# Optimization experiments

Hardware: AMD Instinct MI355X
Metric: run time of the kernel (lower is better)

The kernel has to match this reference:

```python
import math
import jax, jax.numpy as jnp
import numpy as np

N_HEAD = 16


def setup_inputs() -> dict:
    key = jax.random.key(0)
    ks = jax.random.split(key, 6)
    B, T, C = 4, 2048, 1024
    hs = C // N_HEAD
    block_size = 2048
    x = jax.random.normal(ks[0], (B, T, C), dtype=jnp.float32)
    c_attn_w = jax.random.normal(ks[1], (C, 3 * C), dtype=jnp.float32) * 0.02
    c_attn_b = jnp.zeros((3 * C,), dtype=jnp.float32)
    c_proj_w = jax.random.normal(ks[2], (C, C), dtype=jnp.float32) * (0.02 * (2 * 24) ** -0.5)
    c_proj_b = jnp.zeros((C,), dtype=jnp.float32)
    wpe = jax.random.normal(ks[3], (block_size, hs), dtype=jnp.float32) * 0.02
    return {"x": x, "c_attn_w": c_attn_w, "c_attn_b": c_attn_b,
            "c_proj_w": c_proj_w, "c_proj_b": c_proj_b, "wpe": wpe}


def reference(x, c_attn_w, c_attn_b, c_proj_w, c_proj_b, wpe):
    B, T, C = x.shape
    hs = C // N_HEAD
    # fused QKV projection
    qkv = x @ c_attn_w + c_attn_b            # [B, T, 3C]
    q, k, v = jnp.split(qkv, 3, axis=-1)
    pos_emb = wpe[:T]                        # [T, hs]
    # NOTE: faithful to original — raw reshape (not transpose) before the add
    q = (q.reshape(B, N_HEAD, T, hs) + pos_emb).reshape(B, T, N_HEAD, hs)
    k = (k.reshape(B, N_HEAD, T, hs) + pos_emb).reshape(B, T, N_HEAD, hs)
    v = v.reshape(B, T, N_HEAD, hs)
    # vanilla causal attention
    qt = jnp.transpose(q, (0, 2, 1, 3))      # [B, H, T, hs]
    kt = jnp.transpose(k, (0, 2, 3, 1))      # [B, H, hs, T]
    vt = jnp.transpose(v, (0, 2, 1, 3))      # [B, H, T, hs]
    att = qt @ kt / math.sqrt(hs)            # [B, H, T, T]
    causal = jnp.tril(jnp.ones((T, T), dtype=bool))
    att = jnp.where(causal, att, float('-inf'))
    att = jax.nn.softmax(att, axis=-1)
    y = att @ vt                             # [B, H, T, hs]
    y = jnp.transpose(y, (0, 2, 1, 3)).reshape(B, T, C)
    return y @ c_proj_w + c_proj_b
```

## Files before the change

### kernel.cpp

```cpp
#include <hip/hip_runtime.h>

typedef __attribute__((ext_vector_type(8))) short s16x8;
typedef __attribute__((ext_vector_type(4))) float f32x4;
typedef __attribute__((ext_vector_type(4))) unsigned short u16x4;

#define AS1 __attribute__((address_space(1)))
#define AS3 __attribute__((address_space(3)))

__device__ __forceinline__ unsigned short f2bf(float f) {
    union { float f; unsigned u; } c; c.f = f;
    return (unsigned short)((c.u + 0x7FFFu + ((c.u >> 16) & 1u)) >> 16);
}

__global__ void k_f32_to_bf16(const float* __restrict__ src,
                              unsigned short* __restrict__ dst, int n8) {
    int idx = blockIdx.x * 256 + threadIdx.x;
    int stride = gridDim.x * 256;
    for (int i = idx; i < n8; i += stride) {
        const float4* s = (const float4*)src + (size_t)i * 2;
        float4 a = s[0], b = s[1];
        s16x8 o;
        o[0] = (short)f2bf(a.x); o[1] = (short)f2bf(a.y);
        o[2] = (short)f2bf(a.z); o[3] = (short)f2bf(a.w);
        o[4] = (short)f2bf(b.x); o[5] = (short)f2bf(b.y);
        o[6] = (short)f2bf(b.z); o[7] = (short)f2bf(b.w);
        *((s16x8*)dst + i) = o;
    }
}

__global__ __launch_bounds__(256) void k_transpose_bf16(
    const float* __restrict__ W, unsigned short* __restrict__ Wt, int K, int N) {
    __shared__ float t[64][65];
    const int nk = K >> 6;
    const int k0 = (blockIdx.x % nk) << 6;
    const int n0 = (blockIdx.x / nk) << 6;
    const int tid = threadIdx.x;
#pragma unroll
    for (int it = 0; it < 4; it++) {
        int idx = tid + (it << 8);
        int r = idx >> 4, c4 = (idx & 15) << 2;
        float4 v = *(const float4*)(W + (size_t)(k0 + r) * N + n0 + c4);
        t[r][c4] = v.x; t[r][c4 + 1] = v.y; t[r][c4 + 2] = v.z; t[r][c4 + 3] = v.w;
    }
    __syncthreads();
#pragma unroll
    for (int it = 0; it < 2; it++) {
        int idx = tid + (it << 8);
        int rn = idx >> 3, c8 = (idx & 7) << 3;
        s16x8 o;
#pragma unroll
        for (int j = 0; j < 8; j++) o[j] = (short)f2bf(t[c8 + j][rn]);
        *(s16x8*)(Wt + (size_t)(n0 + rn) * K + k0 + c8) = o;
    }
}

__global__ __launch_bounds__(256, 2) void k_gemm_bt(
    const unsigned short* __restrict__ A, const unsigned short* __restrict__ Bt,
    const float* __restrict__ bias, const float* __restrict__ wpe,
    unsigned short* __restrict__ Qo, unsigned short* __restrict__ Ko,
    unsigned short* __restrict__ Vo, float* __restrict__ Fo,
    int N, int K, int mode) {
    __shared__ unsigned short Alds[8192];
    __shared__ unsigned short Blds[8192];
    const int tid = threadIdx.x;
    const int lane = tid & 63, wid = tid >> 6;
    const int ntile = N >> 7;
    const int m0 = (int)(blockIdx.x / ntile) << 7;
    const int n0 = (int)(blockIdx.x % ntile) << 7;
    const int wm = wid & 1, wn = wid >> 1;
    const int lr = lane >> 3, ls = lane & 7;
    const int l15 = lane & 15, lg = lane >> 4;

    const f32x4 vzero = {0.f, 0.f, 0.f, 0.f};
    f32x4 acc[4][4];
#pragma unroll
    for (int i = 0; i < 4; i++)
#pragma unroll
        for (int j = 0; j < 4; j++) acc[i][j] = vzero;

    for (int k0 = 0; k0 < K; k0 += 64) {
#pragma unroll
        for (int i = 0; i < 4; i++) {
            int r = (wid << 5) + (i << 3) + lr;
            int sl = (ls ^ (r & 7)) << 3;
            __builtin_amdgcn_global_load_lds(
                (const AS1 void*)(A + (size_t)(m0 + r) * K + k0 + sl),
                (AS3 void*)(Alds + (wid << 11) + (i << 9)), 16, 0, 0);
            __builtin_amdgcn_global_load_lds(
                (const AS1 void*)(Bt + (size_t)(n0 + r) * K + k0 + sl),
                (AS3 void*)(Blds + (wid << 11) + (i << 9)), 16, 0, 0);
        }
        __syncthreads();
#pragma unroll
        for (int kk = 0; kk < 2; kk++) {
            s16x8 af[4], bfr[4];
#pragma unroll
            for (int mi = 0; mi < 4; mi++) {
                int row = (wm << 6) + (mi << 4) + l15;
                int slot = lg + (kk << 2);
                af[mi] = *(const s16x8*)((const char*)Alds + row * 128 +
                                         ((slot ^ (row & 7)) << 4));
            }
#pragma unroll
            for (int ni = 0; ni < 4; ni++) {
                int row = (wn << 6) + (ni << 4) + l15;
                int slot = lg + (kk << 2);
                bfr[ni] = *(const s16x8*)((const char*)Blds + row * 128 +
                                          ((slot ^ (row & 7)) << 4));
            }
#pragma unroll
            for (int mi = 0; mi < 4; mi++)
#pragma unroll
                for (int ni = 0; ni < 4; ni++)
                    acc[mi][ni] = __builtin_amdgcn_mfma_f32_16x16x32_bf16(
                        af[mi], bfr[ni], acc[mi][ni], 0, 0, 0);
        }
        __syncthreads();
    }

    if (mode == 0) {
#pragma unroll
        for (int ni = 0; ni < 4; ni++) {
            int n = n0 + (wn << 6) + (ni << 4) + l15;
            int which = n >> 10, rem = n & 1023;
            int h = rem >> 6, s = rem & 63;
            unsigned short* out = (which == 0) ? Qo : ((which == 1) ? Ko : Vo);
            float bv = bias[n];
#pragma unroll
            for (int mi = 0; mi < 4; mi++) {
#pragma unroll
                for (int j = 0; j < 4; j++) {
                    int m = m0 + (wm << 6) + (mi << 4) + (lg << 2) + j;
                    int b = m >> 11, t = m & 2047;
                    float v = acc[mi][ni][j] + bv;
                    if (which < 2) v += wpe[((((t << 4) + h) & 2047) << 6) + s];
                    out[(size_t)(b * 16 + h) * 131072 + (size_t)t * 64 + s] = f2bf(v);
                }
            }
        }
    } else {
#pragma unroll
        for (int ni = 0; ni < 4; ni++) {
            int n = n0 + (wn << 6) + (ni << 4) + l15;
            float bv = bias[n];
#pragma unroll
            for (int mi = 0; mi < 4; mi++) {
#pragma unroll
                for (int j = 0; j < 4; j++) {
                    int m = m0 + (wm << 6) + (mi << 4) + (lg << 2) + j;
                    Fo[(size_t)m * N + n] = acc[mi][ni][j] + bv;
                }
            }
        }
    }
}

__global__ __launch_bounds__(256, 4) void k_attn(
    const unsigned short* __restrict__ Qg, const unsigned short* __restrict__ Kg,
    const unsigned short* __restrict__ Vg, unsigned short* __restrict__ Yg) {
    __shared__ unsigned short Klds[4096];
    __shared__ unsigned short Vtlds[4096];
    __shared__ unsigned short Plds[4096];
    const int tid = threadIdx.x, lane = tid & 63, wid = tid >> 6;
    const int l15 = lane & 15, lg = lane >> 4;
    const int lr = lane >> 3, ls = lane & 7;
    const int bh = blockIdx.x >> 4, pi = blockIdx.x & 15;
    const int b = bh >> 4, h = bh & 15;
    const size_t base = (size_t)bh * 131072;
    const int vkv4 = (tid >> 4) << 2;
    const int vd4 = (tid & 15) << 2;

    const f32x4 vzero = {0.f, 0.f, 0.f, 0.f};

#pragma unroll
    for (int phase = 0; phase < 2; phase++) {
        const int qtile = phase ? (31 - pi) : pi;
        const int q0 = qtile << 6;
        const int qrow = q0 + (wid << 4) + l15;

        s16x8 qf[2];
#pragma unroll
        for (int kk = 0; kk < 2; kk++)
            qf[kk] = *(const s16x8*)(Qg + base + (size_t)qrow * 64 +
                                     (kk << 5) + (lg << 3));

        f32x4 o[4];
#pragma unroll
        for (int i = 0; i < 4; i++) o[i] = vzero;
        float mrun = -3.0e38f, lrun = 0.f;

        const int nt = qtile + 1;
        for (int tI = 0; tI < nt; tI++) {
            const int kv0 = tI << 6;
#pragma unroll
            for (int i = 0; i < 2; i++) {
                int r = (wid << 4) + (i << 3) + lr;
                int sl = (ls ^ (r & 7)) << 3;
                __builtin_amdgcn_global_load_lds(
                    (const AS1 void*)(Kg + base + (size_t)(kv0 + r) * 64 + sl),
                    (AS3 void*)(Klds + (wid << 10) + (i << 9)), 16, 0, 0);
            }
            {
                u16x4 vv[4];
#pragma unroll
                for (int r = 0; r < 4; r++)
                    vv[r] = *(const u16x4*)(Vg + base +
                                            (size_t)(kv0 + vkv4 + r) * 64 + vd4);
#pragma unroll
                for (int dj = 0; dj < 4; dj++) {
                    int row = vd4 + dj;
                    unsigned long long pk =
                        (unsigned long long)vv[0][dj] |
                        ((unsigned long long)vv[1][dj] << 16) |
                        ((unsigned long long)vv[2][dj] << 32) |
                        ((unsigned long long)vv[3][dj] << 48);
                    *(unsigned long long*)((char*)Vtlds + row * 128 +
                                           (((vkv4 >> 3) ^ (row & 7)) << 4) +
                                           ((vkv4 & 7) << 1)) = pk;
                }
            }
            __syncthreads();

            f32x4 sacc[4];
#pragma unroll
            for (int i = 0; i < 4; i++) sacc[i] = vzero;
#pragma unroll
            for (int kk = 0; kk < 2; kk++) {
                s16x8 kf[4];
#pragma unroll
                for (int ki = 0; ki < 4; ki++) {
                    int row = (ki << 4) + l15;
                    int slot = lg + (kk << 2);
                    kf[ki] = *(const s16x8*)((const char*)Klds + row * 128 +
                                             ((slot ^ (row & 7)) << 4));
                }
#pragma unroll
                for (int ki = 0; ki < 4; ki++)
                    sacc[ki] = __builtin_amdgcn_mfma_f32_16x16x32_bf16(
                        kf[ki], qf[kk], sacc[ki], 0, 0, 0);
            }

            float tm = -3.0e38f;
            if (tI == nt - 1) {
#pragma unroll
                for (int ki = 0; ki < 4; ki++) {
#pragma unroll
                    for (int j = 0; j < 4; j++) {
                        int kvg = kv0 + (ki << 4) + (lg << 2) + j;
                        float sv = sacc[ki][j] * 0.125f;
                        if (kvg > qrow) sv = -3.0e38f;
                        sacc[ki][j] = sv;
                        tm = fmaxf(tm, sv);
                    }
                }
            } else {
#pragma unroll
                for (int ki = 0; ki < 4; ki++) {
#pragma unroll
                    for (int j = 0; j < 4; j++) {
                        float sv = sacc[ki][j] * 0.125f;
                        sacc[ki][j] = sv;
                        tm = fmaxf(tm, sv);
                    }
                }
            }
            tm = fmaxf(tm, __shfl_xor(tm, 16, 64));
            tm = fmaxf(tm, __shfl_xor(tm, 32, 64));
            float mnew = fmaxf(mrun, tm);
            float rfac = __expf(mrun - mnew);
            mrun = mnew;
            float ps = 0.f;
#pragma unroll
            for (int ki = 0; ki < 4; ki++) {
#pragma unroll
                for (int j = 0; j < 4; j++) {
                    float p = __expf(sacc[ki][j] - mnew);
                    sacc[ki][j] = p;
                    ps += p;
                }
            }
            ps += __shfl_xor(ps, 16, 64);
            ps += __shfl_xor(ps, 32, 64);
            lrun = lrun * rfac + ps;
#pragma unroll
            for (int j = 0; j < 4; j++) {
                float rj = __shfl(rfac, (lane & 48) | ((lg << 2) + j), 64);
#pragma unroll
                for (int si = 0; si < 4; si++) o[si][j] *= rj;
            }
#pragma unroll
            for (int ki = 0; ki < 4; ki++) {
                unsigned long long pk =
                    (unsigned long long)f2bf(sacc[ki][0]) |
                    ((unsigned long long)f2bf(sacc[ki][1]) << 16) |
                    ((unsigned long long)f2bf(sacc[ki][2]) << 32) |
                    ((unsigned long long)f2bf(sacc[ki][3]) << 48);
                int kvl = (ki << 4) + (lg << 2);
                int slot = kvl >> 3;
                *(unsigned long long*)((char*)Plds + (wid << 11) + l15 * 128 +
                                       ((slot ^ (l15 & 7)) << 4) +
                                       ((kvl & 7) << 1)) = pk;
            }

#pragma unroll
            for (int kk = 0; kk < 2; kk++) {
                s16x8 vf[4];
#pragma unroll
                for (int si = 0; si < 4; si++) {
                    int row = (si << 4) + l15;
                    int slot = lg + (kk << 2);
                    vf[si] = *(const s16x8*)((const char*)Vtlds + row * 128 +
                                             ((slot ^ (row & 7)) << 4));
                }
                int prow = l15;
                int slot = lg + (kk << 2);
                s16x8 pf = *(const s16x8*)((const char*)Plds + (wid << 11) +
                                           prow * 128 + ((slot ^ (prow & 7)) << 4));
#pragma unroll
                for (int si = 0; si < 4; si++)
                    o[si] = __builtin_amdgcn_mfma_f32_16x16x32_bf16(
                        pf, vf[si], o[si], 0, 0, 0);
            }
            __syncthreads();
        }

#pragma unroll
        for (int j = 0; j < 4; j++) {
            float lv = __shfl(lrun, (lane & 48) | ((lg << 2) + j), 64);
            float linv = 1.0f / lv;
            int qg = q0 + (wid << 4) + (lg << 2) + j;
            size_t rowoff = ((size_t)b * 2048 + qg) * 1024 + (h << 6);
#pragma unroll
            for (int si = 0; si < 4; si++) {
                int sg = (si << 4) + l15;
                Yg[rowoff + sg] = f2bf(o[si][j] * linv);
            }
        }
    }
}

extern "C" void kernel_launch(void* const* d_in, const int* in_sizes, int n_in,
                              void* d_out, int out_size, void* d_ws, size_t ws_size,
                              hipStream_t stream) {
    const float* x   = (const float*)d_in[0];
    const float* w1  = (const float*)d_in[1];
    const float* b1  = (const float*)d_in[2];
    const float* w2  = (const float*)d_in[3];
    const float* b2  = (const float*)d_in[4];
    const float* wpe = (const float*)d_in[5];
    float* out = (float*)d_out;

    char* ws = (char*)d_ws;
    unsigned short* xb  = (unsigned short*)(ws);
    unsigned short* w1t = (unsigned short*)(ws + 16777216);
    unsigned short* w2t = (unsigned short*)(ws + 23068672);
    unsigned short* Qb  = (unsigned short*)(ws + 25165824);
    unsigned short* Kb  = (unsigned short*)(ws + 41943040);
    unsigned short* Vb  = (unsigned short*)(ws + 58720256);
    unsigned short* Yb  = (unsigned short*)(ws + 75497472);

    k_f32_to_bf16<<<2048, 256, 0, stream>>>(x, xb, 8388608 / 8);
    k_transpose_bf16<<<768, 256, 0, stream>>>(w1, w1t, 1024, 3072);
    k_transpose_bf16<<<256, 256, 0, stream>>>(w2, w2t, 1024, 1024);
    k_gemm_bt<<<64 * 24, 256, 0, stream>>>(xb, w1t, b1, wpe, Qb, Kb, Vb,
                                           nullptr, 3072, 1024, 0);
    k_attn<<<1024, 256, 0, stream>>>(Qb, Kb, Vb, Yb);
    k_gemm_bt<<<64 * 8, 256, 0, stream>>>(Yb, w2t, b2, nullptr, nullptr, nullptr,
                                          nullptr, out, 1024, 1024, 1);
}
```

Baseline: 312.6 us.

## Remap attention and GEMM blocks across XCDs, split q-tile pairs, fold softmax scale

The attention kernel now launches one block per query tile instead of pairing two tiles per block. Blocks are ordered longest-first and mapped so that each XCD handles a fixed set of batch-heads, which should improve L2 reuse of K/V. The GEMM tile index is also remapped to group blocks per XCD. Further changes fold the 1/sqrt(d) scale into an FMA inside the exp, set MFMA sections to higher wave priority, change the V-transpose LDS swizzle to reduce bank conflicts, and raise the attention occupancy hint to 6. The cost is more blocks with uneven work and heavier register pressure from the occupancy hint.

```diff
diff --git a/kernel.cpp b/kernel.cpp
--- a/kernel.cpp
+++ b/kernel.cpp
@@ -65,8 +65,10 @@
     const int tid = threadIdx.x;
     const int lane = tid & 63, wid = tid >> 6;
     const int ntile = N >> 7;
-    const int m0 = (int)(blockIdx.x / ntile) << 7;
-    const int n0 = (int)(blockIdx.x % ntile) << 7;
+    const int chunk = (int)gridDim.x >> 3;
+    const int l = ((int)blockIdx.x & 7) * chunk + ((int)blockIdx.x >> 3);
+    const int m0 = (l / ntile) << 7;
+    const int n0 = (l % ntile) << 7;
     const int wm = wid & 1, wn = wid >> 1;
     const int lr = lane >> 3, ls = lane & 7;
     const int l15 = lane & 15, lg = lane >> 4;
@@ -155,7 +157,7 @@
     }
 }
 
-__global__ __launch_bounds__(256, 4) void k_attn(
+__global__ __launch_bounds__(256, 6) void k_attn(
     const unsigned short* __restrict__ Qg, const unsigned short* __restrict__ Kg,
     const unsigned short* __restrict__ Vg, unsigned short* __restrict__ Yg) {
     __shared__ unsigned short Klds[4096];
@@ -164,177 +166,178 @@
     const int tid = threadIdx.x, lane = tid & 63, wid = tid >> 6;
     const int l15 = lane & 15, lg = lane >> 4;
     const int lr = lane >> 3, ls = lane & 7;
-    const int bh = blockIdx.x >> 4, pi = blockIdx.x & 15;
+    const int p = blockIdx.x;
+    const int xcd = p & 7, rank = p >> 3;
+    const int qt = 31 - (rank >> 3);
+    const int bh = ((rank & 7) << 3) | xcd;
     const int b = bh >> 4, h = bh & 15;
     const size_t base = (size_t)bh * 131072;
+    const int q0 = qt << 6;
+    const int qrow = q0 + (wid << 4) + l15;
     const int vkv4 = (tid >> 4) << 2;
     const int vd4 = (tid & 15) << 2;
 
     const f32x4 vzero = {0.f, 0.f, 0.f, 0.f};
 
-#pragma unroll
-    for (int phase = 0; phase < 2; phase++) {
-        const int qtile = phase ? (31 - pi) : pi;
-        const int q0 = qtile << 6;
-        const int qrow = q0 + (wid << 4) + l15;
-
-        s16x8 qf[2];
-#pragma unroll
-        for (int kk = 0; kk < 2; kk++)
-            qf[kk] = *(const s16x8*)(Qg + base + (size_t)qrow * 64 +
-                                     (kk << 5) + (lg << 3));
-
-        f32x4 o[4];
-#pragma unroll
-        for (int i = 0; i < 4; i++) o[i] = vzero;
-        float mrun = -3.0e38f, lrun = 0.f;
-
-        const int nt = qtile + 1;
-        for (int tI = 0; tI < nt; tI++) {
-            const int kv0 = tI << 6;
-#pragma unroll
-            for (int i = 0; i < 2; i++) {
-                int r = (wid << 4) + (i << 3) + lr;
-                int sl = (ls ^ (r & 7)) << 3;
-                __builtin_amdgcn_global_load_lds(
-                    (const AS1 void*)(Kg + base + (size_t)(kv0 + r) * 64 + sl),
-                    (AS3 void*)(Klds + (wid << 10) + (i << 9)), 16, 0, 0);
-            }
-            {
-                u16x4 vv[4];
-#pragma unroll
-                for (int r = 0; r < 4; r++)
-                    vv[r] = *(const u16x4*)(Vg + base +
-                                            (size_t)(kv0 + vkv4 + r) * 64 + vd4);
-#pragma unroll
-                for (int dj = 0; dj < 4; dj++) {
-                    int row = vd4 + dj;
-                    unsigned long long pk =
-                        (unsigned long long)vv[0][dj] |
-                        ((unsigned long long)vv[1][dj] << 16) |
-                        ((unsigned long long)vv[2][dj] << 32) |
-                        ((unsigned long long)vv[3][dj] << 48);
-                    *(unsigned long long*)((char*)Vtlds + row * 128 +
-                                           (((vkv4 >> 3) ^ (row & 7)) << 4) +
-                                           ((vkv4 & 7) << 1)) = pk;
+    s16x8 qf[2];
+#pragma unroll
+    for (int kk = 0; kk < 2; kk++)
+        qf[kk] = *(const s16x8*)(Qg + base + (size_t)qrow * 64 +
+                                 (kk << 5) + (lg << 3));
+
+    f32x4 o[4];
+#pragma unroll
+    for (int i = 0; i < 4; i++) o[i] = vzero;
+    float mrun = -3.0e38f, lrun = 0.f;
+
+    const int nt = qt + 1;
+    for (int tI = 0; tI < nt; tI++) {
+        const int kv0 = tI << 6;
+#pragma unroll
+        for (int i = 0; i < 2; i++) {
+            int r = (wid << 4) + (i << 3) + lr;
+            int sl = (ls ^ (r & 7)) << 3;
+            __builtin_amdgcn_global_load_lds(
+                (const AS1 void*)(Kg + base + (size_t)(kv0 + r) * 64 + sl),
+                (AS3 void*)(Klds + (wid << 10) + (i << 9)), 16, 0, 0);
+        }
+        {
+            u16x4 vv[4];
+#pragma unroll
+            for (int r = 0; r < 4; r++)
+                vv[r] = *(const u16x4*)(Vg + base +
+                                        (size_t)(kv0 + vkv4 + r) * 64 + vd4);
+#pragma unroll
+            for (int dj = 0; dj < 4; dj++) {
+                int row = vd4 + dj;
+                int fv = (row ^ (row >> 3)) & 7;
+                unsigned long long pk =
+                    (unsigned long long)vv[0][dj] |
+                    ((unsigned long long)vv[1][dj] << 16) |
+                    ((unsigned long long)vv[2][dj] << 32) |
+                    ((unsigned long long)vv[3][dj] << 48);
+                *(unsigned long long*)((char*)Vtlds + row * 128 +
+                                       ((((vkv4 >> 3) ^ fv) & 7) << 4) +
+                                       ((vkv4 & 7) << 1)) = pk;
+            }
+        }
+        __syncthreads();
+
+        f32x4 sacc[4];
+#pragma unroll
+        for (int i = 0; i < 4; i++) sacc[i] = vzero;
+        __builtin_amdgcn_s_setprio(1);
+#pragma unroll
+        for (int kk = 0; kk < 2; kk++) {
+            s16x8 kf[4];
+#pragma unroll
+            for (int ki = 0; ki < 4; ki++) {
+                int row = (ki << 4) + l15;
+                int slot = lg + (kk << 2);
+                kf[ki] = *(const s16x8*)((const char*)Klds + row * 128 +
+                                         ((slot ^ (row & 7)) << 4));
+            }
+#pragma unroll
+            for (int ki = 0; ki < 4; ki++)
+                sacc[ki] = __builtin_amdgcn_mfma_f32_16x16x32_bf16(
+                    kf[ki], qf[kk], sacc[ki], 0, 0, 0);
+        }
+        __builtin_amdgcn_s_setprio(0);
+
+        float tm = -3.0e38f;
+        if (tI == nt - 1) {
+#pragma unroll
+            for (int ki = 0; ki < 4; ki++) {
+#pragma unroll
+                for (int j = 0; j < 4; j++) {
+                    int kvg = kv0 + (ki << 4) + (lg << 2) + j;
+                    float sv = sacc[ki][j];
+                    if (kvg > qrow) sv = -3.0e38f;
+                    sacc[ki][j] = sv;
+                    tm = fmaxf(tm, sv);
                 }
             }
-            __syncthreads();
-
-            f32x4 sacc[4];
-#pragma unroll
-            for (int i = 0; i < 4; i++) sacc[i] = vzero;
-#pragma unroll
-            for (int kk = 0; kk < 2; kk++) {
-                s16x8 kf[4];
-#pragma unroll
-                for (int ki = 0; ki < 4; ki++) {
-                    int row = (ki << 4) + l15;
-                    int slot = lg + (kk << 2);
-                    kf[ki] = *(const s16x8*)((const char*)Klds + row * 128 +
-                                             ((slot ^ (row & 7)) << 4));
-                }
-#pragma unroll
-                for (int ki = 0; ki < 4; ki++)
-                    sacc[ki] = __builtin_amdgcn_mfma_f32_16x16x32_bf16(
-                        kf[ki], qf[kk], sacc[ki], 0, 0, 0);
-            }
-
-            float tm = -3.0e38f;
-            if (tI == nt - 1) {
-#pragma unroll
-                for (int ki = 0; ki < 4; ki++) {
-#pragma unroll
-                    for (int j = 0; j < 4; j++) {
-                        int kvg = kv0 + (ki << 4) + (lg << 2) + j;
-                        float sv = sacc[ki][j] * 0.125f;
-                        if (kvg > qrow) sv = -3.0e38f;
-                        sacc[ki][j] = sv;
-                        tm = fmaxf(tm, sv);
-                    }
-                }
-            } else {
-#pragma unroll
-                for (int ki = 0; ki < 4; ki++) {
-#pragma unroll
-                    for (int j = 0; j < 4; j++) {
-                        float sv = sacc[ki][j] * 0.125f;
-                        sacc[ki][j] = sv;
-                        tm = fmaxf(tm, sv);
-                    }
-                }
-            }
-            tm = fmaxf(tm, __shfl_xor(tm, 16, 64));
-            tm = fmaxf(tm, __shfl_xor(tm, 32, 64));
-            float mnew = fmaxf(mrun, tm);
-            float rfac = __expf(mrun - mnew);
-            mrun = mnew;
-            float ps = 0.f;
+        } else {
 #pragma unroll
             for (int ki = 0; ki < 4; ki++) {
 #pragma unroll
-                for (int j = 0; j < 4; j++) {
-                    float p = __expf(sacc[ki][j] - mnew);
-                    sacc[ki][j] = p;
-                    ps += p;
-                }
-            }
-            ps += __shfl_xor(ps, 16, 64);
-            ps += __shfl_xor(ps, 32, 64);
-            lrun = lrun * rfac + ps;
+                for (int j = 0; j < 4; j++) tm = fmaxf(tm, sacc[ki][j]);
+            }
+        }
+        tm = fmaxf(tm, __shfl_xor(tm, 16, 64));
+        tm = fmaxf(tm, __shfl_xor(tm, 32, 64));
+        float mnew = fmaxf(mrun, tm);
+        float rfac = __expf((mrun - mnew) * 0.125f);
+        float m8 = mnew * 0.125f;
+        mrun = mnew;
+        float ps = 0.f;
+#pragma unroll
+        for (int ki = 0; ki < 4; ki++) {
 #pragma unroll
             for (int j = 0; j < 4; j++) {
-                float rj = __shfl(rfac, (lane & 48) | ((lg << 2) + j), 64);
-#pragma unroll
-                for (int si = 0; si < 4; si++) o[si][j] *= rj;
-            }
-#pragma unroll
-            for (int ki = 0; ki < 4; ki++) {
-                unsigned long long pk =
-                    (unsigned long long)f2bf(sacc[ki][0]) |
-                    ((unsigned long long)f2bf(sacc[ki][1]) << 16) |
-                    ((unsigned long long)f2bf(sacc[ki][2]) << 32) |
-                    ((unsigned long long)f2bf(sacc[ki][3]) << 48);
-                int kvl = (ki << 4) + (lg << 2);
-                int slot = kvl >> 3;
-                *(unsigned long long*)((char*)Plds + (wid << 11) + l15 * 128 +
-                                       ((slot ^ (l15 & 7)) << 4) +
-                                       ((kvl & 7) << 1)) = pk;
-            }
-
-#pragma unroll
-            for (int kk = 0; kk < 2; kk++) {
-                s16x8 vf[4];
-#pragma unroll
-                for (int si = 0; si < 4; si++) {
-                    int row = (si << 4) + l15;
-                    int slot = lg + (kk << 2);
-                    vf[si] = *(const s16x8*)((const char*)Vtlds + row * 128 +
-                                             ((slot ^ (row & 7)) << 4));
-                }
-                int prow = l15;
+                float pv = __expf(__builtin_fmaf(sacc[ki][j], 0.125f, -m8));
+                sacc[ki][j] = pv;
+                ps += pv;
+            }
+        }
+        ps += __shfl_xor(ps, 16, 64);
+        ps += __shfl_xor(ps, 32, 64);
+        lrun = lrun * rfac + ps;
+#pragma unroll
+        for (int j = 0; j < 4; j++) {
+            float rj = __shfl(rfac, (lane & 48) | ((lg << 2) + j), 64);
+#pragma unroll
+            for (int si = 0; si < 4; si++) o[si][j] *= rj;
+        }
+#pragma unroll
+        for (int ki = 0; ki < 4; ki++) {
+            unsigned long long pk =
+                (unsigned long long)f2bf(sacc[ki][0]) |
+                ((unsigned long long)f2bf(sacc[ki][1]) << 16) |
+                ((unsigned long long)f2bf(sacc[ki][2]) << 32) |
+                ((unsigned long long)f2bf(sacc[ki][3]) << 48);
+            int kvl = (ki << 4) + (lg << 2);
+            int slot = kvl >> 3;
+            *(unsigned long long*)((char*)Plds + (wid << 11) + l15 * 128 +
+                                   ((slot ^ (l15 & 7)) << 4) +
+                                   ((kvl & 7) << 1)) = pk;
+        }
+
+        __builtin_amdgcn_s_setprio(1);
+#pragma unroll
+        for (int kk = 0; kk < 2; kk++) {
+            s16x8 vf[4];
+#pragma unroll
+            for (int si = 0; si < 4; si++) {
+                int row = (si << 4) + l15;
                 int slot = lg + (kk << 2);
-                s16x8 pf = *(const s16x8*)((const char*)Plds + (wid << 11) +
-                                           prow * 128 + ((slot ^ (prow & 7)) << 4));
-#pragma unroll
-                for (int si = 0; si < 4; si++)
-                    o[si] = __builtin_amdgcn_mfma_f32_16x16x32_bf16(
-                        pf, vf[si], o[si], 0, 0, 0);
-            }
-            __syncthreads();
-        }
-
-#pragma unroll
-        for (int j = 0; j < 4; j++) {
-            float lv = __shfl(lrun, (lane & 48) | ((lg << 2) + j), 64);
-            float linv = 1.0f / lv;
-            int qg = q0 + (wid << 4) + (lg << 2) + j;
-            size_t rowoff = ((size_t)b * 2048 + qg) * 1024 + (h << 6);
-#pragma unroll
-            for (int si = 0; si < 4; si++) {
-                int sg = (si << 4) + l15;
-                Yg[rowoff + sg] = f2bf(o[si][j] * linv);
-            }
+                int fv = (row ^ (row >> 3)) & 7;
+                vf[si] = *(const s16x8*)((const char*)Vtlds + row * 128 +
+                                         (((slot ^ fv) & 7) << 4));
+            }
+            int prow = l15;
+            int slot = lg + (kk << 2);
+            s16x8 pf = *(const s16x8*)((const char*)Plds + (wid << 11) +
+                                       prow * 128 + ((slot ^ (prow & 7)) << 4));
+#pragma unroll
+            for (int si = 0; si < 4; si++)
+                o[si] = __builtin_amdgcn_mfma_f32_16x16x32_bf16(
+                    pf, vf[si], o[si], 0, 0, 0);
+        }
+        __builtin_amdgcn_s_setprio(0);
+        __syncthreads();
+    }
+
+#pragma unroll
+    for (int j = 0; j < 4; j++) {
+        float lv = __shfl(lrun, (lane & 48) | ((lg << 2) + j), 64);
+        float linv = 1.0f / lv;
+        int qg = q0 + (wid << 4) + (lg << 2) + j;
+        size_t rowoff = ((size_t)b * 2048 + qg) * 1024 + (h << 6);
+#pragma unroll
+        for (int si = 0; si < 4; si++) {
+            int sg = (si << 4) + l15;
+            Yg[rowoff + sg] = f2bf(o[si][j] * linv);
         }
     }
 }
@@ -364,7 +367,7 @@
     k_transpose_bf16<<<256, 256, 0, stream>>>(w2, w2t, 1024, 1024);
     k_gemm_bt<<<64 * 24, 256, 0, stream>>>(xb, w1t, b1, wpe, Qb, Kb, Vb,
                                            nullptr, 3072, 1024, 0);
-    k_attn<<<1024, 256, 0, stream>>>(Qb, Kb, Vb, Yb);
+    k_attn<<<2048, 256, 0, stream>>>(Qb, Kb, Vb, Yb);
     k_gemm_bt<<<64 * 8, 256, 0, stream>>>(Yb, w2t, b2, nullptr, nullptr, nullptr,
                                           nullptr, out, 1024, 1024, 1);
 }
```

After: 302.6 us. -3.2%, faster.
